# Optimization experiments

Measured on AMD Instinct MI355X. Metric: run time of the kernel, lower is better.

The kernel has to match this reference:

```python
import jax, jax.numpy as jnp
import numpy as np
import math

B, S, H, KVH, D, L = 2, 2048, 16, 8, 128, 3
HID = H * D            # 2048 = hidden_size
IN = 2 * HID           # 4096 = q/k/v proj input dim


def rotate_half(x):
    x1 = x[..., : x.shape[-1] // 2]
    x2 = x[..., x.shape[-1] // 2 :]
    return jnp.concatenate((-x2, x1), axis=-1)


def setup_inputs() -> dict:
    key = jax.random.key(0)
    ks = jax.random.split(key, 8)
    hidden_states = jax.random.normal(ks[0], (B, S, IN), jnp.float32)
    # real rotary embeddings (Qwen/LLaMA style)
    inv_freq = 1.0 / (10000.0 ** (jnp.arange(0, D, 2, dtype=jnp.float32) / D))
    freqs = jnp.arange(S, dtype=jnp.float32)[:, None] * inv_freq[None, :]  # [S, D/2]
    emb = jnp.concatenate([freqs, freqs], axis=-1)                          # [S, D]
    cos = jnp.broadcast_to(jnp.cos(emb)[None], (B, S, D)).astype(jnp.float32)
    sin = jnp.broadcast_to(jnp.sin(emb)[None], (B, S, D)).astype(jnp.float32)
    # causal additive mask for the first (full) cache block
    causal = jnp.tril(jnp.ones((S, S), dtype=bool))
    attention_mask = jnp.where(causal, 0.0, -1e9).astype(jnp.float32)
    attention_mask = jnp.broadcast_to(attention_mask[None, None], (B, 1, S, S))
    # stacked tree-cache (already post-repeat_kv: full H heads)
    cache_k = jax.random.normal(ks[1], (L, B, H, S, D), jnp.float32)
    cache_v = jax.random.normal(ks[2], (L, B, H, S, D), jnp.float32)
    Wq = 0.02 * jax.random.normal(ks[3], (HID, IN), jnp.float32)
    Wk = 0.02 * jax.random.normal(ks[4], (KVH * D, IN), jnp.float32)
    Wv = 0.02 * jax.random.normal(ks[5], (KVH * D, IN), jnp.float32)
    Wo = 0.02 * jax.random.normal(ks[6], (HID, HID), jnp.float32)
    return {
        "hidden_states": hidden_states,
        "attention_mask": attention_mask,
        "cos": cos,
        "sin": sin,
        "cache_k": cache_k,
        "cache_v": cache_v,
        "Wq": Wq,
        "Wk": Wk,
        "Wv": Wv,
        "Wo": Wo,
    }


def reference(hidden_states, attention_mask, cos, sin, cache_k, cache_v, Wq, Wk, Wv, Wo):
    bsz, q_len, _ = hidden_states.shape
    scale = 1.0 / math.sqrt(D)
    # projections ([B,S,IN] x [out,IN]^T)
    q = (hidden_states @ Wq.T).reshape(bsz, q_len, H, D).transpose(0, 2, 1, 3)    # [B,H,S,D]
    k = (hidden_states @ Wk.T).reshape(bsz, q_len, KVH, D).transpose(0, 2, 1, 3)  # [B,KVH,S,D]
    v = (hidden_states @ Wv.T).reshape(bsz, q_len, KVH, D).transpose(0, 2, 1, 3)
    # RoPE (cos/sin unsqueezed at head dim)
    c = cos[:, None]  # [B,1,S,D]
    s = sin[:, None]
    q = q * c + rotate_half(q) * s
    k = k * c + rotate_half(k) * s
    # GQA repeat (matches torch expand+reshape ordering)
    n_rep = H // KVH
    k = jnp.repeat(k, n_rep, axis=1)  # [B,H,S,D]
    v = jnp.repeat(v, n_rep, axis=1)
    # tree-cache: full attention vs step-0 cache, diagonal vs later steps + current
    k0, v0 = cache_k[0], cache_v[0]
    extra_k = jnp.concatenate([cache_k[1:], k[None]], axis=0)  # [L,B,H,S,D]
    extra_v = jnp.concatenate([cache_v[1:], v[None]], axis=0)
    w0 = jnp.einsum("bhqd,bhkd->bhqk", q, k0) * scale + attention_mask      # [B,H,S,S]
    we = jnp.einsum("bhsd,lbhsd->bhsl", q, extra_k) * scale                 # [B,H,S,L]
    w = jnp.concatenate([w0, we], axis=-1)
    w = jax.nn.softmax(w.astype(jnp.float32), axis=-1).astype(q.dtype)
    out = jnp.einsum("bhqk,bhkd->bhqd", w[..., :q_len], v0)
    out = out + jnp.einsum("bhsl,lbhsd->bhsd", w[..., q_len:], extra_v)
    out = out.transpose(0, 2, 1, 3).reshape(bsz, q_len, HID)
    return out @ Wo.T
```

## Files before the change

kernel.cpp:

```cpp
#include <hip/hip_runtime.h>

typedef unsigned int u32;
typedef unsigned short u16;
typedef __attribute__((ext_vector_type(8))) short bf16x8;
typedef __attribute__((ext_vector_type(4))) float f32x4;

#define B_   2
#define S_   2048
#define H_   16
#define KVH_ 8
#define D_   128
#define HID_ 2048
#define IN_  4096

__device__ __forceinline__ float bf2f(short h) {
    return __builtin_bit_cast(float, (u32)((u16)h) << 16);
}
__device__ __forceinline__ u16 f2bf(float f) {
    u32 u = __builtin_bit_cast(u32, f);
    u += 0x7FFF + ((u >> 16) & 1);
    return (u16)(u >> 16);
}

__device__ __forceinline__ void gl_lds16(const void* g, void* l) {
    __builtin_amdgcn_global_load_lds(
        (const __attribute__((address_space(1))) u32*)g,
        (__attribute__((address_space(3))) u32*)l, 16, 0, 0);
}

__device__ __forceinline__ f32x4 mfma16(bf16x8 a, bf16x8 b, f32x4 c) {
    return __builtin_amdgcn_mfma_f32_16x16x32_bf16(a, b, c, 0, 0, 0);
}

__global__ void k_conv(const float* __restrict__ s, u16* __restrict__ d, int n4) {
    int i = blockIdx.x * 256 + threadIdx.x;
    if (i < n4) {
        float4 v = ((const float4*)s)[i];
        ushort4 o;
        o.x = f2bf(v.x); o.y = f2bf(v.y); o.z = f2bf(v.z); o.w = f2bf(v.w);
        ((ushort4*)d)[i] = o;
    }
}

__global__ void k_vtrans(const float* __restrict__ src, u16* __restrict__ dst) {
    __shared__ float t[32][33];
    const int bh = blockIdx.z, d0 = blockIdx.y * 32, s0 = blockIdx.x * 32;
    const int tx = threadIdx.x & 31, ty = threadIdx.x >> 5;
    const float* sp = src + (size_t)bh * S_ * D_;
#pragma unroll
    for (int i = 0; i < 4; i++) {
        int sl = ty + i * 8;
        t[tx][sl] = sp[(size_t)(s0 + sl) * D_ + d0 + tx];
    }
    __syncthreads();
    u16* dp = dst + (size_t)bh * D_ * S_;
#pragma unroll
    for (int i = 0; i < 4; i++) {
        int dl = ty + i * 8;
        dp[(size_t)(d0 + dl) * S_ + s0 + tx] = f2bf(t[dl][tx]);
    }
}

__global__ void k_rope(u16* __restrict__ Q0, u16* __restrict__ Kn,
                       const float* __restrict__ cosp, const float* __restrict__ sinp) {
    int idx = blockIdx.x * 256 + threadIdx.x;
    const float scale = 0.08838834764831845f;
    if (idx < B_ * H_ * S_ * 64) {
        int d = idx & 63, s = (idx >> 6) & (S_ - 1), bh = idx >> 17;
        int b = bh >> 4;
        u16* base = Q0 + ((size_t)bh * S_ + s) * D_;
        size_t ci = ((size_t)(b * S_ + s)) * D_ + d;
        float c = cosp[ci], sn = sinp[ci];
        float x1 = bf2f((short)base[d]), x2 = bf2f((short)base[d + 64]);
        base[d]      = f2bf((x1 * c - x2 * sn) * scale);
        base[d + 64] = f2bf((x2 * c + x1 * sn) * scale);
    } else {
        int t2 = idx - B_ * H_ * S_ * 64;
        int d = t2 & 63, s = (t2 >> 6) & (S_ - 1), bh = t2 >> 17;
        int b = bh >> 3;
        u16* base = Kn + ((size_t)bh * S_ + s) * D_;
        size_t ci = ((size_t)(b * S_ + s)) * D_ + d;
        float c = cosp[ci], sn = sinp[ci];
        float x1 = bf2f((short)base[d]), x2 = bf2f((short)base[d + 64]);
        base[d]      = f2bf(x1 * c - x2 * sn);
        base[d + 64] = f2bf(x2 * c + x1 * sn);
    }
}

template <int EPI>
__global__ __launch_bounds__(256) void k_gemm(
    const u16* __restrict__ A, const u16* __restrict__ Bm,
    float* __restrict__ Cf, u16* __restrict__ q0p, u16* __restrict__ knp,
    u16* __restrict__ vnp, int M, int N, int K) {
    __shared__ __align__(16) u16 Ash[128 * 32];
    __shared__ __align__(16) u16 Bsh[128 * 32];
    const int tid = threadIdx.x;
    const int w = tid >> 6, lane = tid & 63, quad = lane >> 4, l15 = lane & 15;
    const int m0 = blockIdx.y * 128, n0 = blockIdx.x * 128;
    const int wm = (w >> 1) * 64, wn = (w & 1) * 64;

    f32x4 acc[4][4];
#pragma unroll
    for (int i = 0; i < 4; i++)
#pragma unroll
        for (int j = 0; j < 4; j++) acc[i][j] = (f32x4){0.f, 0.f, 0.f, 0.f};

    int pA = tid, pB = tid + 256;
    int ar0 = pA >> 2, akc0 = (pA & 3) ^ ((ar0 >> 1) & 3);
    int ar1 = pB >> 2, akc1 = (pB & 3) ^ ((ar1 >> 1) & 3);
    const u16* Ag0 = A + (size_t)(m0 + ar0) * K + akc0 * 8;
    const u16* Ag1 = A + (size_t)(m0 + ar1) * K + akc1 * 8;
    const u16* Bg0 = Bm + (size_t)(n0 + ar0) * K + akc0 * 8;
    const u16* Bg1 = Bm + (size_t)(n0 + ar1) * K + akc1 * 8;
    u16* lA0 = Ash + (w * 64) * 8;
    u16* lA1 = Ash + (256 + w * 64) * 8;
    u16* lB0 = Bsh + (w * 64) * 8;
    u16* lB1 = Bsh + (256 + w * 64) * 8;

    for (int k0 = 0; k0 < K; k0 += 32) {
        gl_lds16(Ag0 + k0, lA0);
        gl_lds16(Ag1 + k0, lA1);
        gl_lds16(Bg0 + k0, lB0);
        gl_lds16(Bg1 + k0, lB1);
        __syncthreads();
        bf16x8 af[4], bfr[4];
#pragma unroll
        for (int mi = 0; mi < 4; mi++) {
            int m = wm + mi * 16 + l15;
            af[mi] = *(const bf16x8*)(Ash + (m * 4 + (quad ^ ((m >> 1) & 3))) * 8);
        }
#pragma unroll
        for (int ni = 0; ni < 4; ni++) {
            int n = wn + ni * 16 + l15;
            bfr[ni] = *(const bf16x8*)(Bsh + (n * 4 + (quad ^ ((n >> 1) & 3))) * 8);
        }
#pragma unroll
        for (int mi = 0; mi < 4; mi++)
#pragma unroll
            for (int ni = 0; ni < 4; ni++)
                acc[mi][ni] = mfma16(af[mi], bfr[ni], acc[mi][ni]);
        __syncthreads();
    }

    if constexpr (EPI == 0) {
#pragma unroll
        for (int mi = 0; mi < 4; mi++)
#pragma unroll
            for (int ni = 0; ni < 4; ni++) {
                int nn = n0 + wn + ni * 16 + l15;
#pragma unroll
                for (int reg = 0; reg < 4; reg++) {
                    int mm = m0 + wm + mi * 16 + quad * 4 + reg;
                    Cf[(size_t)mm * N + nn] = acc[mi][ni][reg];
                }
            }
    } else {
#pragma unroll
        for (int mi = 0; mi < 4; mi++)
#pragma unroll
            for (int ni = 0; ni < 4; ni++) {
                int nn = n0 + wn + ni * 16 + l15;
#pragma unroll
                for (int reg = 0; reg < 4; reg++) {
                    int mm = m0 + wm + mi * 16 + quad * 4 + reg;
                    int bb = mm >> 11, ss = mm & (S_ - 1);
                    u16 val = f2bf(acc[mi][ni][reg]);
                    if (nn < 2048) {
                        q0p[(((size_t)(bb * H_ + (nn >> 7))) * S_ + ss) * D_ + (nn & 127)] = val;
                    } else if (nn < 3072) {
                        knp[(((size_t)(bb * KVH_ + ((nn - 2048) >> 7))) * S_ + ss) * D_ + (nn & 127)] = val;
                    } else {
                        vnp[(((size_t)(bb * KVH_ + ((nn - 3072) >> 7))) * S_ + ss) * D_ + (nn & 127)] = val;
                    }
                }
            }
    }
}

__global__ __launch_bounds__(256) void k_attn(
    const u16* __restrict__ Q0, const u16* __restrict__ K0c, const u16* __restrict__ V0T,
    const u16* __restrict__ Kn, const u16* __restrict__ Vn,
    const float* __restrict__ ck, const float* __restrict__ cv,
    u16* __restrict__ AO) {
    __shared__ __align__(16) u16 Ksh[4096];
    __shared__ __align__(16) u16 VTsh[4096];
    __shared__ __align__(16) u16 Psh[4 * 16 * 40];
    __shared__ float esh[4 * 48];
    const int tid = threadIdx.x, w = tid >> 6, lane = tid & 63;
    const int quad = lane >> 4, l15 = lane & 15;
    const int b = blockIdx.z, h = blockIdx.y, q0 = blockIdx.x * 64;
    const int bh = b * H_ + h;
    const size_t kbase = (size_t)bh * S_ * D_;

    bf16x8 qf[4];
    {
        const u16* qp = Q0 + kbase + (size_t)(q0 + w * 16 + l15) * D_;
#pragma unroll
        for (int t = 0; t < 4; t++) qf[t] = *(const bf16x8*)(qp + t * 32 + quad * 8);
    }
    f32x4 Ot[8];
#pragma unroll
    for (int t = 0; t < 8; t++) Ot[t] = (f32x4){0.f, 0.f, 0.f, 0.f};
    float mrow[4] = {-1e30f, -1e30f, -1e30f, -1e30f};
    float lrow[4] = {0.f, 0.f, 0.f, 0.f};

    int pA = tid, pB = tid + 256;
    int kj0 = pA >> 4, kc0 = (pA & 15) ^ ((kj0 >> 1) & 7);
    int kj1 = pB >> 4, kc1 = (pB & 15) ^ ((kj1 >> 1) & 7);
    int vd0 = pA >> 2, vq0 = (pA & 3) ^ ((vd0 >> 1) & 3);
    int vd1 = pB >> 2, vq1 = (pB & 3) ^ ((vd1 >> 1) & 3);
    const u16* kg0 = K0c + kbase + (size_t)kj0 * D_ + kc0 * 8;
    const u16* kg1 = K0c + kbase + (size_t)kj1 * D_ + kc1 * 8;
    const u16* vg0 = V0T + kbase + (size_t)vd0 * S_ + vq0 * 8;
    const u16* vg1 = V0T + kbase + (size_t)vd1 * S_ + vq1 * 8;
    u16* lk0 = Ksh + (w * 64) * 8;
    u16* lk1 = Ksh + (256 + w * 64) * 8;
    u16* lv0 = VTsh + (w * 64) * 8;
    u16* lv1 = VTsh + (256 + w * 64) * 8;

    const int ntiles = (q0 >> 5) + 2;
    for (int jt = 0; jt < ntiles; ++jt) {
        const int j0 = jt * 32;
        gl_lds16(kg0 + (size_t)j0 * D_, lk0);
        gl_lds16(kg1 + (size_t)j0 * D_, lk1);
        gl_lds16(vg0 + j0, lv0);
        gl_lds16(vg1 + j0, lv1);
        __syncthreads();

        f32x4 s0 = (f32x4){0.f, 0.f, 0.f, 0.f}, s1 = (f32x4){0.f, 0.f, 0.f, 0.f};
#pragma unroll
        for (int t = 0; t < 4; t++) {
            int kc = t * 4 + quad;
            bf16x8 k0f = *(const bf16x8*)(Ksh + (l15 * 16 + (kc ^ ((l15 >> 1) & 7))) * 8);
            int j1i = l15 + 16;
            bf16x8 k1f = *(const bf16x8*)(Ksh + (j1i * 16 + (kc ^ ((j1i >> 1) & 7))) * 8);
            s0 = mfma16(qf[t], k0f, s0);
            s1 = mfma16(qf[t], k1f, s1);
        }
        if (j0 + 31 > q0 + w * 16) {
#pragma unroll
            for (int reg = 0; reg < 4; reg++) {
                int r = q0 + w * 16 + quad * 4 + reg;
                if (j0 + l15 > r) s0[reg] = -1e30f;
                if (j0 + 16 + l15 > r) s1[reg] = -1e30f;
            }
        }
        float pr0[4], pr1[4], alpha[4];
#pragma unroll
        for (int reg = 0; reg < 4; reg++) {
            float tm = fmaxf(s0[reg], s1[reg]);
            tm = fmaxf(tm, __shfl_xor(tm, 1));
            tm = fmaxf(tm, __shfl_xor(tm, 2));
            tm = fmaxf(tm, __shfl_xor(tm, 4));
            tm = fmaxf(tm, __shfl_xor(tm, 8));
            float mn = fmaxf(mrow[reg], tm);
            alpha[reg] = __expf(mrow[reg] - mn);
            mrow[reg] = mn;
            pr0[reg] = __expf(s0[reg] - mn);
            pr1[reg] = __expf(s1[reg] - mn);
            float rs = pr0[reg] + pr1[reg];
            rs += __shfl_xor(rs, 1);
            rs += __shfl_xor(rs, 2);
            rs += __shfl_xor(rs, 4);
            rs += __shfl_xor(rs, 8);
            lrow[reg] = lrow[reg] * alpha[reg] + rs;
        }
#pragma unroll
        for (int t = 0; t < 8; t++)
#pragma unroll
            for (int reg = 0; reg < 4; reg++) Ot[t][reg] *= alpha[reg];

        u16* pb = Psh + w * 640;
#pragma unroll
        for (int reg = 0; reg < 4; reg++) {
            int r = quad * 4 + reg;
            pb[r * 40 + l15] = f2bf(pr0[reg]);
            pb[r * 40 + 16 + l15] = f2bf(pr1[reg]);
        }
        bf16x8 pa = *(const bf16x8*)(pb + l15 * 40 + quad * 8);
#pragma unroll
        for (int t = 0; t < 8; t++) {
            int d = t * 16 + l15;
            bf16x8 vb = *(const bf16x8*)(VTsh + (d * 4 + (quad ^ ((d >> 1) & 3))) * 8);
            Ot[t] = mfma16(pa, vb, Ot[t]);
        }
        __syncthreads();
    }

    const int srow_a = q0 + w * 16 + l15;
    float ev[3];
#pragma unroll
    for (int c = 0; c < 2; c++) {
        const float* kp = ck + ((size_t)((1 + c) * B_ + b) * H_ + h) * S_ * D_ + (size_t)srow_a * D_;
        float part = 0.f;
#pragma unroll
        for (int t = 0; t < 4; t++) {
            int dbase = t * 32 + quad * 8;
            float4 v0 = *(const float4*)(kp + dbase);
            float4 v1 = *(const float4*)(kp + dbase + 4);
            part += bf2f(qf[t][0]) * v0.x + bf2f(qf[t][1]) * v0.y +
                    bf2f(qf[t][2]) * v0.z + bf2f(qf[t][3]) * v0.w;
            part += bf2f(qf[t][4]) * v1.x + bf2f(qf[t][5]) * v1.y +
                    bf2f(qf[t][6]) * v1.z + bf2f(qf[t][7]) * v1.w;
        }
        part += __shfl_xor(part, 16);
        part += __shfl_xor(part, 32);
        ev[c] = part;
    }
    {
        const u16* kp = Kn + ((size_t)(b * KVH_ + (h >> 1)) * S_ + srow_a) * D_;
        float part = 0.f;
#pragma unroll
        for (int t = 0; t < 4; t++) {
            bf16x8 kv = *(const bf16x8*)(kp + t * 32 + quad * 8);
#pragma unroll
            for (int i = 0; i < 8; i++) part += bf2f(qf[t][i]) * bf2f(kv[i]);
        }
        part += __shfl_xor(part, 16);
        part += __shfl_xor(part, 32);
        ev[2] = part;
    }
    if (quad == 0) {
        esh[w * 48 + l15] = ev[0];
        esh[w * 48 + 16 + l15] = ev[1];
        esh[w * 48 + 32 + l15] = ev[2];
    }
    __syncthreads();

    float alr[4], w0r[4], w1r[4], w2r[4], invr[4];
#pragma unroll
    for (int reg = 0; reg < 4; reg++) {
        int r = quad * 4 + reg;
        float e0 = esh[w * 48 + r], e1 = esh[w * 48 + 16 + r], e2 = esh[w * 48 + 32 + r];
        float mn = fmaxf(fmaxf(mrow[reg], e0), fmaxf(e1, e2));
        alr[reg] = __expf(mrow[reg] - mn);
        w0r[reg] = __expf(e0 - mn);
        w1r[reg] = __expf(e1 - mn);
        w2r[reg] = __expf(e2 - mn);
        float lf = lrow[reg] * alr[reg] + w0r[reg] + w1r[reg] + w2r[reg];
        invr[reg] = 1.f / lf;
    }
    const float* v1p = cv + ((size_t)(B_ + b) * H_ + h) * S_ * D_;
    const float* v2p = cv + ((size_t)(2 * B_ + b) * H_ + h) * S_ * D_;
    const u16* vnp = Vn + ((size_t)(b * KVH_ + (h >> 1))) * S_ * D_;
#pragma unroll
    for (int t = 0; t < 8; t++) {
        int d = t * 16 + l15;
#pragma unroll
        for (int reg = 0; reg < 4; reg++) {
            int sr = q0 + w * 16 + quad * 4 + reg;
            float v1 = v1p[(size_t)sr * D_ + d];
            float v2 = v2p[(size_t)sr * D_ + d];
            float vn = bf2f((short)vnp[(size_t)sr * D_ + d]);
            float o = (Ot[t][reg] * alr[reg] + w0r[reg] * v1 + w1r[reg] * v2 + w2r[reg] * vn) * invr[reg];
            AO[((size_t)(b * S_ + sr)) * HID_ + h * D_ + d] = f2bf(o);
        }
    }
}

extern "C" void kernel_launch(void* const* d_in, const int* in_sizes, int n_in,
                              void* d_out, int out_size, void* d_ws, size_t ws_size,
                              hipStream_t stream) {
    const float* hs      = (const float*)d_in[0];
    const float* cosp    = (const float*)d_in[2];
    const float* sinp    = (const float*)d_in[3];
    const float* cache_k = (const float*)d_in[4];
    const float* cache_v = (const float*)d_in[5];
    const float* Wq      = (const float*)d_in[6];
    const float* Wk      = (const float*)d_in[7];
    const float* Wv      = (const float*)d_in[8];
    const float* Wo      = (const float*)d_in[9];
    float* out = (float*)d_out;

    u16* ws = (u16*)d_ws;
    u16* X16  = ws;
    u16* AO   = ws;
    u16* Wqkv = ws + 16777216;
    u16* K0c  = ws + 16777216;
    u16* V0T  = ws + 25165824;
    u16* Wo16 = ws + 33554432;
    u16* Q0   = ws + 37748736;
    u16* Kn   = ws + 46137344;
    u16* Vn   = ws + 50331648;

    k_conv<<<16384, 256, 0, stream>>>(hs, X16, 4194304);
    k_conv<<<8192, 256, 0, stream>>>(Wq, Wqkv, 2097152);
    k_conv<<<4096, 256, 0, stream>>>(Wk, Wqkv + 8388608, 1048576);
    k_conv<<<4096, 256, 0, stream>>>(Wv, Wqkv + 12582912, 1048576);
    k_conv<<<4096, 256, 0, stream>>>(Wo, Wo16, 1048576);

    k_gemm<1><<<dim3(32, 32), 256, 0, stream>>>(X16, Wqkv, nullptr, Q0, Kn, Vn,
                                                4096, 4096, 4096);
    k_rope<<<24576, 256, 0, stream>>>(Q0, Kn, cosp, sinp);

    k_conv<<<8192, 256, 0, stream>>>(cache_k, K0c, 2097152);
    k_vtrans<<<dim3(64, 4, 32), 256, 0, stream>>>(cache_v, V0T);

    k_attn<<<dim3(32, 16, 2), 256, 0, stream>>>(Q0, K0c, V0T, Kn, Vn,
                                                cache_k, cache_v, AO);
    k_gemm<0><<<dim3(16, 32), 256, 0, stream>>>(AO, Wo16, out, nullptr, nullptr,
                                                nullptr, 4096, 2048, 2048);
}
```

Measured before the change: 830.3 us.

## Double-buffer attention K/V tiles, reorder blocks, swizzle GEMM tiles, fuse weight conversions

The attention kernel now double-buffers its K and V^T LDS tiles, prefetching the next tile while the current one is computed, and synchronises with explicit waitcnt and barrier. It skips rescaling the accumulator when no row maximum grows, and defers the row-sum reduction to the end. The grid is remapped so the longest causal query blocks launch first. The GEMM uses a grouped block swizzle for L2 reuse, and the four weight conversion kernels are merged into one launch. This doubles LDS use in attention and adds branches, which may reduce occupancy.

```diff
diff --git a/kernel.cpp b/kernel.cpp
--- a/kernel.cpp
+++ b/kernel.cpp
@@ -40,6 +40,22 @@
         o.x = f2bf(v.x); o.y = f2bf(v.y); o.z = f2bf(v.z); o.w = f2bf(v.w);
         ((ushort4*)d)[i] = o;
     }
+}
+
+__global__ void k_convw(const float* __restrict__ wq, const float* __restrict__ wk,
+                        const float* __restrict__ wv, const float* __restrict__ wo,
+                        u16* __restrict__ dq, u16* __restrict__ dk,
+                        u16* __restrict__ dv, u16* __restrict__ dwo) {
+    int i = blockIdx.x * 256 + threadIdx.x;
+    const float* s; u16* d; int off;
+    if (i < 2097152)      { s = wq; d = dq;  off = i; }
+    else if (i < 3145728) { s = wk; d = dk;  off = i - 2097152; }
+    else if (i < 4194304) { s = wv; d = dv;  off = i - 3145728; }
+    else                  { s = wo; d = dwo; off = i - 4194304; }
+    float4 v = ((const float4*)s)[off];
+    ushort4 o;
+    o.x = f2bf(v.x); o.y = f2bf(v.y); o.z = f2bf(v.z); o.w = f2bf(v.w);
+    ((ushort4*)d)[off] = o;
 }
 
 __global__ void k_vtrans(const float* __restrict__ src, u16* __restrict__ dst) {
@@ -96,7 +112,11 @@
     __shared__ __align__(16) u16 Bsh[128 * 32];
     const int tid = threadIdx.x;
     const int w = tid >> 6, lane = tid & 63, quad = lane >> 4, l15 = lane & 15;
-    const int m0 = blockIdx.y * 128, n0 = blockIdx.x * 128;
+    const int lin = blockIdx.y * gridDim.x + blockIdx.x;
+    const int gmsz = 8 * gridDim.x;
+    const int grp = lin / gmsz, rem = lin % gmsz;
+    const int m0 = (grp * 8 + (rem & 7)) * 128;
+    const int n0 = (rem >> 3) * 128;
     const int wm = (w >> 1) * 64, wn = (w & 1) * 64;
 
     f32x4 acc[4][4];
@@ -182,13 +202,14 @@
     const u16* __restrict__ Kn, const u16* __restrict__ Vn,
     const float* __restrict__ ck, const float* __restrict__ cv,
     u16* __restrict__ AO) {
-    __shared__ __align__(16) u16 Ksh[4096];
-    __shared__ __align__(16) u16 VTsh[4096];
+    __shared__ __align__(16) u16 Ksh[2 * 4096];
+    __shared__ __align__(16) u16 VTsh[2 * 4096];
     __shared__ __align__(16) u16 Psh[4 * 16 * 40];
     __shared__ float esh[4 * 48];
     const int tid = threadIdx.x, w = tid >> 6, lane = tid & 63;
     const int quad = lane >> 4, l15 = lane & 15;
-    const int b = blockIdx.z, h = blockIdx.y, q0 = blockIdx.x * 64;
+    const int b = blockIdx.x >> 4, h = blockIdx.x & 15;
+    const int q0 = (31 - blockIdx.y) * 64;
     const int bh = b * H_ + h;
     const size_t kbase = (size_t)bh * S_ * D_;
 
@@ -213,27 +234,38 @@
     const u16* kg1 = K0c + kbase + (size_t)kj1 * D_ + kc1 * 8;
     const u16* vg0 = V0T + kbase + (size_t)vd0 * S_ + vq0 * 8;
     const u16* vg1 = V0T + kbase + (size_t)vd1 * S_ + vq1 * 8;
-    u16* lk0 = Ksh + (w * 64) * 8;
-    u16* lk1 = Ksh + (256 + w * 64) * 8;
-    u16* lv0 = VTsh + (w * 64) * 8;
-    u16* lv1 = VTsh + (256 + w * 64) * 8;
+    const int ofsA = w * 512, ofsB = 2048 + w * 512;
 
     const int ntiles = (q0 >> 5) + 2;
+    gl_lds16(kg0, Ksh + ofsA);
+    gl_lds16(kg1, Ksh + ofsB);
+    gl_lds16(vg0, VTsh + ofsA);
+    gl_lds16(vg1, VTsh + ofsB);
+
     for (int jt = 0; jt < ntiles; ++jt) {
+        const int cur = jt & 1;
+        const u16* Kb = Ksh + cur * 4096;
+        const u16* Vb = VTsh + cur * 4096;
+        if (jt + 1 < ntiles) {
+            const int nb = (cur ^ 1) * 4096;
+            const size_t j1 = (size_t)(jt + 1) * 32;
+            gl_lds16(kg0 + j1 * D_, Ksh + nb + ofsA);
+            gl_lds16(kg1 + j1 * D_, Ksh + nb + ofsB);
+            gl_lds16(vg0 + j1, VTsh + nb + ofsA);
+            gl_lds16(vg1 + j1, VTsh + nb + ofsB);
+            __asm__ volatile("s_waitcnt vmcnt(4)\n\ts_barrier" ::: "memory");
+        } else {
+            __asm__ volatile("s_waitcnt vmcnt(0)\n\ts_barrier" ::: "memory");
+        }
         const int j0 = jt * 32;
-        gl_lds16(kg0 + (size_t)j0 * D_, lk0);
-        gl_lds16(kg1 + (size_t)j0 * D_, lk1);
-        gl_lds16(vg0 + j0, lv0);
-        gl_lds16(vg1 + j0, lv1);
-        __syncthreads();
 
         f32x4 s0 = (f32x4){0.f, 0.f, 0.f, 0.f}, s1 = (f32x4){0.f, 0.f, 0.f, 0.f};
 #pragma unroll
         for (int t = 0; t < 4; t++) {
             int kc = t * 4 + quad;
-            bf16x8 k0f = *(const bf16x8*)(Ksh + (l15 * 16 + (kc ^ ((l15 >> 1) & 7))) * 8);
+            bf16x8 k0f = *(const bf16x8*)(Kb + (l15 * 16 + (kc ^ ((l15 >> 1) & 7))) * 8);
             int j1i = l15 + 16;
-            bf16x8 k1f = *(const bf16x8*)(Ksh + (j1i * 16 + (kc ^ ((j1i >> 1) & 7))) * 8);
+            bf16x8 k1f = *(const bf16x8*)(Kb + (j1i * 16 + (kc ^ ((j1i >> 1) & 7))) * 8);
             s0 = mfma16(qf[t], k0f, s0);
             s1 = mfma16(qf[t], k1f, s1);
         }
@@ -246,6 +278,7 @@
             }
         }
         float pr0[4], pr1[4], alpha[4];
+        int changed = 0;
 #pragma unroll
         for (int reg = 0; reg < 4; reg++) {
             float tm = fmaxf(s0[reg], s1[reg]);
@@ -253,22 +286,23 @@
             tm = fmaxf(tm, __shfl_xor(tm, 2));
             tm = fmaxf(tm, __shfl_xor(tm, 4));
             tm = fmaxf(tm, __shfl_xor(tm, 8));
-            float mn = fmaxf(mrow[reg], tm);
-            alpha[reg] = __expf(mrow[reg] - mn);
-            mrow[reg] = mn;
-            pr0[reg] = __expf(s0[reg] - mn);
-            pr1[reg] = __expf(s1[reg] - mn);
-            float rs = pr0[reg] + pr1[reg];
-            rs += __shfl_xor(rs, 1);
-            rs += __shfl_xor(rs, 2);
-            rs += __shfl_xor(rs, 4);
-            rs += __shfl_xor(rs, 8);
-            lrow[reg] = lrow[reg] * alpha[reg] + rs;
-        }
-#pragma unroll
-        for (int t = 0; t < 8; t++)
-#pragma unroll
-            for (int reg = 0; reg < 4; reg++) Ot[t][reg] *= alpha[reg];
+            if (tm > mrow[reg]) {
+                changed = 1;
+                alpha[reg] = __expf(mrow[reg] - tm);
+                mrow[reg] = tm;
+            } else {
+                alpha[reg] = 1.f;
+            }
+            pr0[reg] = __expf(s0[reg] - mrow[reg]);
+            pr1[reg] = __expf(s1[reg] - mrow[reg]);
+            lrow[reg] = lrow[reg] * alpha[reg] + pr0[reg] + pr1[reg];
+        }
+        if (__any(changed)) {
+#pragma unroll
+            for (int t = 0; t < 8; t++)
+#pragma unroll
+                for (int reg = 0; reg < 4; reg++) Ot[t][reg] *= alpha[reg];
+        }
 
         u16* pb = Psh + w * 640;
 #pragma unroll
@@ -281,10 +315,21 @@
 #pragma unroll
         for (int t = 0; t < 8; t++) {
             int d = t * 16 + l15;
-            bf16x8 vb = *(const bf16x8*)(VTsh + (d * 4 + (quad ^ ((d >> 1) & 3))) * 8);
+            bf16x8 vb = *(const bf16x8*)(Vb + (d * 4 + (quad ^ ((d >> 1) & 3))) * 8);
             Ot[t] = mfma16(pa, vb, Ot[t]);
         }
-        __syncthreads();
+        __asm__ volatile("s_barrier" ::: "memory");
+    }
+
+    float lsum[4];
+#pragma unroll
+    for (int reg = 0; reg < 4; reg++) {
+        float r = lrow[reg];
+        r += __shfl_xor(r, 1);
+        r += __shfl_xor(r, 2);
+        r += __shfl_xor(r, 4);
+        r += __shfl_xor(r, 8);
+        lsum[reg] = r;
     }
 
     const int srow_a = q0 + w * 16 + l15;
@@ -337,7 +382,7 @@
         w0r[reg] = __expf(e0 - mn);
         w1r[reg] = __expf(e1 - mn);
         w2r[reg] = __expf(e2 - mn);
-        float lf = lrow[reg] * alr[reg] + w0r[reg] + w1r[reg] + w2r[reg];
+        float lf = lsum[reg] * alr[reg] + w0r[reg] + w1r[reg] + w2r[reg];
         invr[reg] = 1.f / lf;
     }
     const float* v1p = cv + ((size_t)(B_ + b) * H_ + h) * S_ * D_;
@@ -384,10 +429,8 @@
     u16* Vn   = ws + 50331648;
 
     k_conv<<<16384, 256, 0, stream>>>(hs, X16, 4194304);
-    k_conv<<<8192, 256, 0, stream>>>(Wq, Wqkv, 2097152);
-    k_conv<<<4096, 256, 0, stream>>>(Wk, Wqkv + 8388608, 1048576);
-    k_conv<<<4096, 256, 0, stream>>>(Wv, Wqkv + 12582912, 1048576);
-    k_conv<<<4096, 256, 0, stream>>>(Wo, Wo16, 1048576);
+    k_convw<<<20480, 256, 0, stream>>>(Wq, Wk, Wv, Wo,
+                                       Wqkv, Wqkv + 8388608, Wqkv + 12582912, Wo16);
 
     k_gemm<1><<<dim3(32, 32), 256, 0, stream>>>(X16, Wqkv, nullptr, Q0, Kn, Vn,
                                                 4096, 4096, 4096);
@@ -396,8 +439,8 @@
     k_conv<<<8192, 256, 0, stream>>>(cache_k, K0c, 2097152);
     k_vtrans<<<dim3(64, 4, 32), 256, 0, stream>>>(cache_v, V0T);
 
-    k_attn<<<dim3(32, 16, 2), 256, 0, stream>>>(Q0, K0c, V0T, Kn, Vn,
-                                                cache_k, cache_v, AO);
+    k_attn<<<dim3(32, 32), 256, 0, stream>>>(Q0, K0c, V0T, Kn, Vn,
+                                             cache_k, cache_v, AO);
     k_gemm<0><<<dim3(16, 32), 256, 0, stream>>>(AO, Wo16, out, nullptr, nullptr,
                                                 nullptr, 4096, 2048, 2048);
 }
```

New measurement: 713.6 us. -14.0%, faster.
